# Optimization experiments

Hardware: AMD Instinct MI355X
Metric: run time of the kernel (lower is better)

Reference implementation:

```python
import jax, jax.numpy as jnp
import numpy as np

Q = 12          # hidden_features = number of qubits
L = 3           # spectrum_layer
NBLK = 2        # N sequential circuit blocks
IMG = 32        # image side; input_dim = IMG*IMG = 1024
DIM = 1 << Q

# bit table: BITS[s, j] = bit of wire j (wire 0 = most significant) in basis state s
_s = np.arange(DIM)
_BITS_NP = np.stack([(_s >> (Q - 1 - j)) & 1 for j in range(Q)], axis=1).astype(np.float32)
BITS = jnp.asarray(_BITS_NP)                      # (2^Q, Q)
ZVALS = jnp.asarray(1.0 - 2.0 * _BITS_NP)         # PauliZ eigenvalues per wire

def _cz_ring_sign(r):
    # diagonal of a ring of CZ gates on pairs (j, (j+r) % Q); CZ is diagonal, ring commutes
    m = sum(_BITS_NP[:, j] * _BITS_NP[:, (j + r) % Q] for j in range(Q))
    return jnp.asarray(1.0 - 2.0 * (m % 2)).astype(np.float32)

# StronglyEntanglingLayers default ranges for 2 sub-layers: r = (l % (Q-1)) + 1 -> [1, 2]
CZ_SIGNS = [_cz_ring_sign(1), _cz_ring_sign(2)]

def _rot(phi, theta, omega):
    # PennyLane Rot(phi, theta, omega) = RZ(omega) RY(theta) RZ(phi)
    c = jnp.cos(theta * 0.5).astype(jnp.complex64)
    s = jnp.sin(theta * 0.5).astype(jnp.complex64)
    row0 = jnp.stack([jnp.exp(-0.5j * (phi + omega)) * c, -jnp.exp(0.5j * (phi - omega)) * s])
    row1 = jnp.stack([jnp.exp(0.5j * (omega - phi)) * s, jnp.exp(0.5j * (phi + omega)) * c])
    return jnp.stack([row0, row1])  # (2,2) complex64

def _apply_1q(st, U, wire):
    b = st.shape[0]
    left, right = 1 << wire, 1 << (Q - 1 - wire)
    st = st.reshape(b, left, 2, right)
    st = jnp.einsum('ij,bljr->blir', U, st)
    return st.reshape(b, DIM)

def _circuit(inputs, w):
    # inputs: (b, Q) real angles; w: (L, 2, Q, 3)
    b = inputs.shape[0]
    st = jnp.zeros((b, DIM), jnp.complex64).at[:, 0].set(1.0)
    # RZ(theta) = diag(e^{-i t/2}, e^{+i t/2}) on every wire -> one diagonal phase per sample
    enc = jnp.exp(1j * (inputs @ (BITS - 0.5).T)).astype(jnp.complex64)  # (b, 2^Q)
    for i in range(L):
        st = st * enc
        for l in range(2):
            for wire in range(Q):
                st = _apply_1q(st, _rot(w[i, l, wire, 0], w[i, l, wire, 1], w[i, l, wire, 2]), wire)
            st = st * CZ_SIGNS[l]
    probs = st.real * st.real + st.imag * st.imag
    return probs @ ZVALS  # (b, Q) expval PauliZ per wire

def setup_inputs() -> dict:
    key = jax.random.key(0)
    ks = jax.random.split(key, 6)
    return {
        'x': jax.random.normal(ks[0], (2048, 1, IMG, IMG), jnp.float32),
        'conv_w': jax.random.normal(ks[1], (Q, 1, 3, 3), jnp.float32) * 0.3,
        'conv_b': jax.random.normal(ks[2], (Q,), jnp.float32) * 0.1,
        'weights1': jax.random.normal(ks[3], (NBLK, L, 2, Q, 3), jnp.float32) * 0.4,
        'lin_w': jax.random.normal(ks[4], (IMG * IMG, Q), jnp.float32) * 0.2,
        'lin_b': jax.random.normal(ks[5], (IMG * IMG,), jnp.float32) * 0.05,
    }

def reference(x, conv_w, conv_b, weights1, lin_w, lin_b):
    b = x.shape[0]
    y = jax.lax.conv_general_dilated(
        x, conv_w, window_strides=(2, 2), padding=((1, 1), (1, 1)),
        dimension_numbers=('NCHW', 'OIHW', 'NCHW')) + conv_b[None, :, None, None]
    xr = y.reshape(b, Q, -1).mean(axis=2)  # global average pool per channel -> (b, Q)
    for n in range(NBLK):
        xr = _circuit(xr, weights1[n])
    out = xr @ lin_w.T + lin_b
    return out.reshape(b, 1, IMG, IMG)
```

## Files before the change

kernel.cpp:

```cpp
#include <hip/hip_runtime.h>

typedef float vf2  __attribute__((ext_vector_type(2)));
typedef float v128f __attribute__((ext_vector_type(128)));

__device__ __forceinline__ vf2 cmulv(vf2 a, vf2 b){
  vf2 br; br.x = -b.y; br.y = b.x;
  return a.x*b + a.y*br;
}

#define ROWS 66
#define FENCE() asm volatile("" ::: "memory")

#define ALPHA(d, j) (((d) & 1) \
  ? (W[((((d)>>1)*2+1)*12+(j))*3+0] + W[((((d)>>1)*2+0)*12+(j))*3+2]) \
  : (W[((((d)>>1)*2+0)*12+(j))*3+0] + xr[(j)] + W[(((((d)>>1)-1)*2+1)*12+(j))*3+2]))

#define GATES6(sl, par) do{ \
  _Pragma("unroll") \
  for (int lb = 0; lb < 6; lb++){ \
    const int wire_ = (par) ? (5 - lb) : (11 - lb); \
    const float t_ = scsl[(sl)*12 + wire_].y; \
    _Pragma("unroll") \
    for (int w0 = 0; w0 < 64; w0++){ \
      if (w0 & (1 << lb)) continue; \
      const int w1 = w0 | (1 << lb); \
      const float ax_ = st[2*w0], ay_ = st[2*w0+1]; \
      const float bx_ = st[2*w1], by_ = st[2*w1+1]; \
      st[2*w0]   = __builtin_fmaf(-t_, bx_, ax_); \
      st[2*w0+1] = __builtin_fmaf(-t_, by_, ay_); \
      st[2*w1]   = __builtin_fmaf( t_, ax_, bx_); \
      st[2*w1+1] = __builtin_fmaf( t_, ay_, by_); \
    } \
  } \
}while(0)

#define TRANSPOSE() do{ \
  _Pragma("unroll") \
  for (int w = 0; w < 64; w++){ \
    vf2 t_; t_.x = st[2*w]; t_.y = st[2*w+1]; \
    xbuf[w * ROWS + u] = t_; \
  } \
  FENCE(); \
  _Pragma("unroll") \
  for (int j = 0; j < 32; j++){ \
    float4 f_ = ((const float4*)&xbuf[u * ROWS])[j]; \
    st[4*j] = f_.x; st[4*j+1] = f_.y; st[4*j+2] = f_.z; st[4*j+3] = f_.w; \
  } \
  FENCE(); \
}while(0)

#define DIAG(d, par) do{ \
  vf2 lp_ = ltab[(d)-1][u]; \
  vf2 lpn_ = -lp_; \
  const unsigned m_ = (par) ? ( ((u >> 5) & 1u) | ((u & 1u) << 5) ) \
                            : ( (((u >> 1) & 1u) << 5) | ((u & 1u) << 4) \
                              | (((u >> 5) & 1u) << 1) | ((u >> 4) & 1u) ); \
  _Pragma("unroll") \
  for (int w = 0; w < 64; w++){ \
    vf2 dph_ = tabs[(d)-1][w]; \
    const int sx_ = __popc((unsigned)w & m_) & 1; \
    vf2 a_; a_.x = st[2*w]; a_.y = st[2*w+1]; \
    vf2 t_ = cmulv(a_, dph_); \
    vf2 r_ = cmulv(t_, sx_ ? lpn_ : lp_); \
    st[2*w] = r_.x; st[2*w+1] = r_.y; \
  } \
}while(0)

__global__ __attribute__((amdgpu_flat_work_group_size(64,64)))
__attribute__((amdgpu_waves_per_eu(1)))
void qiddm_wave(const float* __restrict__ gx,
                const float* __restrict__ gcw,
                const float* __restrict__ gcb,
                const float* __restrict__ gw1,
                const float* __restrict__ glw,
                const float* __restrict__ glb,
                float* __restrict__ gout)
{
  __shared__ vf2 xbuf[64 * ROWS];
  __shared__ vf2 tabs[5][64];
  __shared__ vf2 ltab[5][64];
  __shared__ vf2 scsl[72];

  const int u = threadIdx.x;
  const int bid = blockIdx.x;

  float xr[12];

  {
    float* img = (float*)xbuf;
#pragma unroll
    for (int i = 0; i < 4; i++){
      float4 q4 = ((const float4*)gx)[(size_t)bid * 256 + i * 64 + u];
      ((float4*)img)[i * 64 + u] = q4;
    }
    float p[4][9];
#pragma unroll
    for (int i = 0; i < 4; i++){
      int pos = u + 64 * i, oi = pos >> 4, oj = pos & 15;
#pragma unroll
      for (int ki = 0; ki < 3; ki++)
#pragma unroll
        for (int kj = 0; kj < 3; kj++){
          int ri = 2*oi - 1 + ki, cj = 2*oj - 1 + kj;
          p[i][ki*3+kj] = (ri >= 0 && ri < 32 && cj >= 0 && cj < 32) ? img[ri*32+cj] : 0.0f;
        }
    }
#pragma unroll
    for (int q = 0; q < 12; q++){
      float a = 0.0f;
#pragma unroll
      for (int e = 0; e < 9; e++){
        float wv = gcw[q*9+e];
#pragma unroll
        for (int i = 0; i < 4; i++) a += p[i][e] * wv;
      }
#pragma unroll
      for (int off = 32; off; off >>= 1) a += __shfl_xor(a, off);
      xr[q] = gcb[q] + a * (1.0f/256.0f);
    }
  }

#pragma unroll 1
  for (int n = 0; n < 2; n++){
    const float* W = gw1 + n * 216;

    float myc = 1.0f;
#pragma unroll
    for (int rep = 0; rep < 2; rep++){
      int e = u + rep * 64;
      if (e < 72){
        float sv, cv; __sincosf(0.5f * W[e*3+1], &sv, &cv);
        vf2 ct; ct.x = cv; ct.y = __fdividef(sv, cv); scsl[e] = ct;
        if (e >= 12) myc *= cv;
      }
    }
#pragma unroll
    for (int off = 32; off; off >>= 1) myc *= __shfl_xor(myc, off);
    const float C2 = myc * myc;

#pragma unroll
    for (int d = 1; d <= 5; d++){
      const int par = d & 1;
      const int r = par ? 1 : 2;
      {
        float ph = 0.0f;
#pragma unroll
        for (int lb = 0; lb < 6; lb++){
          int wire = par ? (5 - lb) : (11 - lb);
          ph += ALPHA(d, wire) * ((float)((u >> lb) & 1) - 0.5f);
        }
        int idx_r = par ? (u << 6) : u;
        int y = ((idx_r << r) | (idx_r >> (12 - r))) & 0xFFF;
        int s = __popc(idx_r & y) & 1;
        float sv, cv; __sincosf(ph, &sv, &cv);
        vf2 e_; e_.x = cv; e_.y = sv; if (s) e_ = -e_;
        tabs[d-1][u] = e_;
      }
      {
        float ph = 0.0f;
#pragma unroll
        for (int lb = 0; lb < 6; lb++){
          int wire = par ? (11 - lb) : (5 - lb);
          ph += ALPHA(d, wire) * ((float)((u >> lb) & 1) - 0.5f);
        }
        int idx_l = par ? u : (u << 6);
        int y = ((idx_l << r) | (idx_l >> (12 - r))) & 0xFFF;
        int s = __popc(idx_l & y) & 1;
        float sv, cv; __sincosf(ph, &sv, &cv);
        vf2 e_; e_.x = cv; e_.y = sv; if (s) e_ = -e_;
        ltab[d-1][u] = e_;
      }
    }
    FENCE();

    v128f st;
    float fl = 1.0f;
#pragma unroll
    for (int lb = 0; lb < 6; lb++){
      vf2 ct = scsl[11 - lb];
      fl *= ((u >> lb) & 1) ? (ct.x * ct.y) : ct.x;
    }
    float qc[6], qs[6];
#pragma unroll
    for (int rb = 0; rb < 6; rb++){
      vf2 ct = scsl[5 - rb]; qc[rb] = ct.x; qs[rb] = ct.x * ct.y;
    }
#pragma unroll
    for (int w = 0; w < 64; w++){
      float Qw =  ((w & 1)  ? qs[0] : qc[0]);
      Qw      *=  ((w & 2)  ? qs[1] : qc[1]);
      Qw      *=  ((w & 4)  ? qs[2] : qc[2]);
      Qw      *=  ((w & 8)  ? qs[3] : qc[3]);
      Qw      *=  ((w & 16) ? qs[4] : qc[4]);
      Qw      *=  ((w & 32) ? qs[5] : qc[5]);
      st[2*w] = fl * Qw; st[2*w+1] = 0.0f;
    }

#pragma unroll 1
    for (int k = 2; k < 12; k++){
      const int sl  = k >> 1;
      const int par = ((k + 1) >> 1) & 1;
      if (k & 1) TRANSPOSE();
      else       DIAG(sl, par);
      GATES6(sl, par);
    }

    {
      float P = 0.f, mm[6] = {0.f,0.f,0.f,0.f,0.f,0.f};
#pragma unroll
      for (int w = 0; w < 64; w++){
        float re = st[2*w], im = st[2*w+1];
        float pr = re*re + im*im;
        P += pr;
#pragma unroll
        for (int i = 0; i < 6; i++)
          mm[i] += ((w >> (5 - i)) & 1) ? -pr : pr;
      }
#pragma unroll
      for (int q = 0; q < 12; q++){
        float val = (q < 6) ? (((u >> (5 - q)) & 1) ? -P : P)
                            : mm[q - 6];
#pragma unroll
        for (int off = 32; off; off >>= 1) val += __shfl_xor(val, off);
        xr[q] = val * C2;
      }
    }
  }

  {
#pragma unroll
    for (int i = 0; i < 16; i++){
      int o = i * 64 + u;
      const float4* wr = (const float4*)(glw + o * 12);
      float4 w0 = wr[0], w1 = wr[1], w2 = wr[2];
      float a = glb[o];
      a += xr[0]*w0.x + xr[1]*w0.y + xr[2]*w0.z + xr[3]*w0.w;
      a += xr[4]*w1.x + xr[5]*w1.y + xr[6]*w1.z + xr[7]*w1.w;
      a += xr[8]*w2.x + xr[9]*w2.y + xr[10]*w2.z + xr[11]*w2.w;
      gout[(size_t)bid * 1024 + o] = a;
    }
  }
}

extern "C" void kernel_launch(void* const* d_in, const int* in_sizes, int n_in,
                              void* d_out, int out_size, void* d_ws, size_t ws_size,
                              hipStream_t stream)
{
  (void)n_in; (void)d_ws; (void)ws_size; (void)out_size;
  const float* x  = (const float*)d_in[0];
  const float* cw = (const float*)d_in[1];
  const float* cb = (const float*)d_in[2];
  const float* w1 = (const float*)d_in[3];
  const float* lw = (const float*)d_in[4];
  const float* lb = (const float*)d_in[5];
  float* out = (float*)d_out;
  const int nb = in_sizes[0] / 1024;
  hipLaunchKernelGGL(qiddm_wave, dim3(nb), dim3(64), 0, stream,
                     x, cw, cb, w1, lw, lb, out);
}
```

Measured before the change: 182.9 us.

## Process two samples per wave and share the sample-independent first circuit stage

Each 64-lane block now simulates two samples (A and B) with two register-resident state vectors, and the grid is halved. The gate stages before the first input-dependent diagonal are the same for both samples, so they are computed once and the state is copied to the second sample. The LDS transpose is split into two half-size buffers, and the phase tables are extended for the second sample. The intent is to cut redundant work and raise instruction-level parallelism, at the cost of doubled register state and fewer waves per CU.

```diff
diff --git a/kernel.cpp b/kernel.cpp
--- a/kernel.cpp
+++ b/kernel.cpp
@@ -11,11 +11,20 @@
 #define ROWS 66
 #define FENCE() asm volatile("" ::: "memory")
 
-#define ALPHA(d, j) (((d) & 1) \
+#define ALPHA(d, j, XR) (((d) & 1) \
   ? (W[((((d)>>1)*2+1)*12+(j))*3+0] + W[((((d)>>1)*2+0)*12+(j))*3+2]) \
-  : (W[((((d)>>1)*2+0)*12+(j))*3+0] + xr[(j)] + W[(((((d)>>1)-1)*2+1)*12+(j))*3+2]))
-
-#define GATES6(sl, par) do{ \
+  : (W[((((d)>>1)*2+0)*12+(j))*3+0] + XR[(j)] + W[(((((d)>>1)-1)*2+1)*12+(j))*3+2]))
+
+#define BFLY(ST, w0i, w1i, t_) do{ \
+  const float ax_=ST[2*(w0i)], ay_=ST[2*(w0i)+1]; \
+  const float bx_=ST[2*(w1i)], by_=ST[2*(w1i)+1]; \
+  ST[2*(w0i)]   = __builtin_fmaf(-(t_), bx_, ax_); \
+  ST[2*(w0i)+1] = __builtin_fmaf(-(t_), by_, ay_); \
+  ST[2*(w1i)]   = __builtin_fmaf( (t_), ax_, bx_); \
+  ST[2*(w1i)+1] = __builtin_fmaf( (t_), ay_, by_); \
+}while(0)
+
+#define GATES6_1(ST, sl, par) do{ \
   _Pragma("unroll") \
   for (int lb = 0; lb < 6; lb++){ \
     const int wire_ = (par) ? (5 - lb) : (11 - lb); \
@@ -24,45 +33,152 @@
     for (int w0 = 0; w0 < 64; w0++){ \
       if (w0 & (1 << lb)) continue; \
       const int w1 = w0 | (1 << lb); \
-      const float ax_ = st[2*w0], ay_ = st[2*w0+1]; \
-      const float bx_ = st[2*w1], by_ = st[2*w1+1]; \
-      st[2*w0]   = __builtin_fmaf(-t_, bx_, ax_); \
-      st[2*w0+1] = __builtin_fmaf(-t_, by_, ay_); \
-      st[2*w1]   = __builtin_fmaf( t_, ax_, bx_); \
-      st[2*w1+1] = __builtin_fmaf( t_, ay_, by_); \
+      BFLY(ST, w0, w1, t_); \
     } \
   } \
 }while(0)
 
-#define TRANSPOSE() do{ \
+#define GATES6_2(sl, par) do{ \
+  _Pragma("unroll") \
+  for (int lb = 0; lb < 6; lb++){ \
+    const int wire_ = (par) ? (5 - lb) : (11 - lb); \
+    const float t_ = scsl[(sl)*12 + wire_].y; \
+    _Pragma("unroll") \
+    for (int w0 = 0; w0 < 64; w0++){ \
+      if (w0 & (1 << lb)) continue; \
+      const int w1 = w0 | (1 << lb); \
+      BFLY(stA, w0, w1, t_); \
+      BFLY(stB, w0, w1, t_); \
+    } \
+  } \
+}while(0)
+
+#define TRANSPOSE_S(ST, XB) do{ \
+  if (u < 32){ \
+    _Pragma("unroll") \
+    for (int w = 32; w < 64; w++){ vf2 t_; t_.x = ST[2*w]; t_.y = ST[2*w+1]; \
+      XB[(w-32) * ROWS + u] = t_; } \
+  } else { \
+    _Pragma("unroll") \
+    for (int w = 0; w < 32; w++){ vf2 t_; t_.x = ST[2*w]; t_.y = ST[2*w+1]; \
+      XB[w * ROWS + u] = t_; } \
+  } \
+  FENCE(); \
+  if (u < 32){ \
+    _Pragma("unroll") \
+    for (int t = 0; t < 16; t++){ \
+      float4 f_ = ((const float4*)&XB[u * ROWS + 32])[t]; \
+      ST[64+4*t] = f_.x; ST[64+4*t+1] = f_.y; ST[64+4*t+2] = f_.z; ST[64+4*t+3] = f_.w; } \
+  } else { \
+    _Pragma("unroll") \
+    for (int t = 0; t < 16; t++){ \
+      float4 f_ = ((const float4*)&XB[(u-32) * ROWS])[t]; \
+      ST[4*t] = f_.x; ST[4*t+1] = f_.y; ST[4*t+2] = f_.z; ST[4*t+3] = f_.w; } \
+  } \
+  FENCE(); \
+  if (u < 32){ \
+    _Pragma("unroll") \
+    for (int w = 0; w < 32; w++){ vf2 t_; t_.x = ST[2*w]; t_.y = ST[2*w+1]; \
+      XB[w * ROWS + u] = t_; } \
+  } else { \
+    _Pragma("unroll") \
+    for (int w = 32; w < 64; w++){ vf2 t_; t_.x = ST[2*w]; t_.y = ST[2*w+1]; \
+      XB[(w-32) * ROWS + u] = t_; } \
+  } \
+  FENCE(); \
+  if (u < 32){ \
+    _Pragma("unroll") \
+    for (int t = 0; t < 16; t++){ \
+      float4 f_ = ((const float4*)&XB[u * ROWS])[t]; \
+      ST[4*t] = f_.x; ST[4*t+1] = f_.y; ST[4*t+2] = f_.z; ST[4*t+3] = f_.w; } \
+  } else { \
+    _Pragma("unroll") \
+    for (int t = 0; t < 16; t++){ \
+      float4 f_ = ((const float4*)&XB[(u-32) * ROWS + 32])[t]; \
+      ST[64+4*t] = f_.x; ST[64+4*t+1] = f_.y; ST[64+4*t+2] = f_.z; ST[64+4*t+3] = f_.w; } \
+  } \
+  FENCE(); \
+}while(0)
+
+#define TRANSPOSE2() do{ \
+  if (u < 32){ \
+    _Pragma("unroll") \
+    for (int w = 32; w < 64; w++){ vf2 tA_, tB_; \
+      tA_.x = stA[2*w]; tA_.y = stA[2*w+1]; xbA[(w-32) * ROWS + u] = tA_; \
+      tB_.x = stB[2*w]; tB_.y = stB[2*w+1]; xbB[(w-32) * ROWS + u] = tB_; } \
+  } else { \
+    _Pragma("unroll") \
+    for (int w = 0; w < 32; w++){ vf2 tA_, tB_; \
+      tA_.x = stA[2*w]; tA_.y = stA[2*w+1]; xbA[w * ROWS + u] = tA_; \
+      tB_.x = stB[2*w]; tB_.y = stB[2*w+1]; xbB[w * ROWS + u] = tB_; } \
+  } \
+  FENCE(); \
+  if (u < 32){ \
+    _Pragma("unroll") \
+    for (int t = 0; t < 16; t++){ \
+      float4 fA_ = ((const float4*)&xbA[u * ROWS + 32])[t]; \
+      float4 fB_ = ((const float4*)&xbB[u * ROWS + 32])[t]; \
+      stA[64+4*t] = fA_.x; stA[64+4*t+1] = fA_.y; stA[64+4*t+2] = fA_.z; stA[64+4*t+3] = fA_.w; \
+      stB[64+4*t] = fB_.x; stB[64+4*t+1] = fB_.y; stB[64+4*t+2] = fB_.z; stB[64+4*t+3] = fB_.w; } \
+  } else { \
+    _Pragma("unroll") \
+    for (int t = 0; t < 16; t++){ \
+      float4 fA_ = ((const float4*)&xbA[(u-32) * ROWS])[t]; \
+      float4 fB_ = ((const float4*)&xbB[(u-32) * ROWS])[t]; \
+      stA[4*t] = fA_.x; stA[4*t+1] = fA_.y; stA[4*t+2] = fA_.z; stA[4*t+3] = fA_.w; \
+      stB[4*t] = fB_.x; stB[4*t+1] = fB_.y; stB[4*t+2] = fB_.z; stB[4*t+3] = fB_.w; } \
+  } \
+  FENCE(); \
+  if (u < 32){ \
+    _Pragma("unroll") \
+    for (int w = 0; w < 32; w++){ vf2 tA_, tB_; \
+      tA_.x = stA[2*w]; tA_.y = stA[2*w+1]; xbA[w * ROWS + u] = tA_; \
+      tB_.x = stB[2*w]; tB_.y = stB[2*w+1]; xbB[w * ROWS + u] = tB_; } \
+  } else { \
+    _Pragma("unroll") \
+    for (int w = 32; w < 64; w++){ vf2 tA_, tB_; \
+      tA_.x = stA[2*w]; tA_.y = stA[2*w+1]; xbA[(w-32) * ROWS + u] = tA_; \
+      tB_.x = stB[2*w]; tB_.y = stB[2*w+1]; xbB[(w-32) * ROWS + u] = tB_; } \
+  } \
+  FENCE(); \
+  if (u < 32){ \
+    _Pragma("unroll") \
+    for (int t = 0; t < 16; t++){ \
+      float4 fA_ = ((const float4*)&xbA[u * ROWS])[t]; \
+      float4 fB_ = ((const float4*)&xbB[u * ROWS])[t]; \
+      stA[4*t] = fA_.x; stA[4*t+1] = fA_.y; stA[4*t+2] = fA_.z; stA[4*t+3] = fA_.w; \
+      stB[4*t] = fB_.x; stB[4*t+1] = fB_.y; stB[4*t+2] = fB_.z; stB[4*t+3] = fB_.w; } \
+  } else { \
+    _Pragma("unroll") \
+    for (int t = 0; t < 16; t++){ \
+      float4 fA_ = ((const float4*)&xbA[(u-32) * ROWS + 32])[t]; \
+      float4 fB_ = ((const float4*)&xbB[(u-32) * ROWS + 32])[t]; \
+      stA[64+4*t] = fA_.x; stA[64+4*t+1] = fA_.y; stA[64+4*t+2] = fA_.z; stA[64+4*t+3] = fA_.w; \
+      stB[64+4*t] = fB_.x; stB[64+4*t+1] = fB_.y; stB[64+4*t+2] = fB_.z; stB[64+4*t+3] = fB_.w; } \
+  } \
+  FENCE(); \
+}while(0)
+
+#define DIAG2(d) do{ \
+  const int par_ = (d) & 1; \
+  vf2 lpA_ = ((d)==2) ? lA[1] : ((d)==3) ? lA[2] : ((d)==4) ? lA[3] : lA[4]; \
+  vf2 lpB_ = ((d)==2) ? lB[1] : ((d)==3) ? lA[2] : ((d)==4) ? lB[3] : lA[4]; \
+  vf2 lpnA_ = -lpA_, lpnB_ = -lpB_; \
+  const vf2* tA_ = &tabs[(d)-1][0]; \
+  const vf2* tB_ = par_ ? tA_ : &tabsE[((d)>>1)-1][0]; \
+  const unsigned m_ = par_ ? ( ((u >> 5) & 1u) | ((u & 1u) << 5) ) \
+                           : ( (((u >> 1) & 1u) << 5) | ((u & 1u) << 4) \
+                             | (((u >> 5) & 1u) << 1) | ((u >> 4) & 1u) ); \
   _Pragma("unroll") \
   for (int w = 0; w < 64; w++){ \
-    vf2 t_; t_.x = st[2*w]; t_.y = st[2*w+1]; \
-    xbuf[w * ROWS + u] = t_; \
-  } \
-  FENCE(); \
-  _Pragma("unroll") \
-  for (int j = 0; j < 32; j++){ \
-    float4 f_ = ((const float4*)&xbuf[u * ROWS])[j]; \
-    st[4*j] = f_.x; st[4*j+1] = f_.y; st[4*j+2] = f_.z; st[4*j+3] = f_.w; \
-  } \
-  FENCE(); \
-}while(0)
-
-#define DIAG(d, par) do{ \
-  vf2 lp_ = ltab[(d)-1][u]; \
-  vf2 lpn_ = -lp_; \
-  const unsigned m_ = (par) ? ( ((u >> 5) & 1u) | ((u & 1u) << 5) ) \
-                            : ( (((u >> 1) & 1u) << 5) | ((u & 1u) << 4) \
-                              | (((u >> 5) & 1u) << 1) | ((u >> 4) & 1u) ); \
-  _Pragma("unroll") \
-  for (int w = 0; w < 64; w++){ \
-    vf2 dph_ = tabs[(d)-1][w]; \
     const int sx_ = __popc((unsigned)w & m_) & 1; \
-    vf2 a_; a_.x = st[2*w]; a_.y = st[2*w+1]; \
-    vf2 t_ = cmulv(a_, dph_); \
-    vf2 r_ = cmulv(t_, sx_ ? lpn_ : lp_); \
-    st[2*w] = r_.x; st[2*w+1] = r_.y; \
+    vf2 dA_ = tA_[w], dB_ = tB_[w]; \
+    { vf2 a_; a_.x = stA[2*w]; a_.y = stA[2*w+1]; \
+      vf2 t_ = cmulv(a_, dA_); vf2 r_ = cmulv(t_, sx_ ? lpnA_ : lpA_); \
+      stA[2*w] = r_.x; stA[2*w+1] = r_.y; } \
+    { vf2 a_; a_.x = stB[2*w]; a_.y = stB[2*w+1]; \
+      vf2 t_ = cmulv(a_, dB_); vf2 r_ = cmulv(t_, sx_ ? lpnB_ : lpB_); \
+      stB[2*w] = r_.x; stB[2*w+1] = r_.y; } \
   } \
 }while(0)
 
@@ -76,24 +192,30 @@
                 const float* __restrict__ glb,
                 float* __restrict__ gout)
 {
-  __shared__ vf2 xbuf[64 * ROWS];
+  __shared__ vf2 xbA[32 * ROWS];
+  __shared__ vf2 xbB[32 * ROWS];
   __shared__ vf2 tabs[5][64];
-  __shared__ vf2 ltab[5][64];
+  __shared__ vf2 tabsE[2][64];
   __shared__ vf2 scsl[72];
 
   const int u = threadIdx.x;
   const int bid = blockIdx.x;
-
-  float xr[12];
+  const int sid0 = bid * 2, sid1 = bid * 2 + 1;
+
+  float xrA[12], xrB[12];
 
   {
-    float* img = (float*)xbuf;
+    float* imgA = (float*)xbA;
+    float* imgB = (float*)xbB;
 #pragma unroll
     for (int i = 0; i < 4; i++){
-      float4 q4 = ((const float4*)gx)[(size_t)bid * 256 + i * 64 + u];
-      ((float4*)img)[i * 64 + u] = q4;
-    }
-    float p[4][9];
+      float4 qA = ((const float4*)gx)[(size_t)sid0 * 256 + i * 64 + u];
+      float4 qB = ((const float4*)gx)[(size_t)sid1 * 256 + i * 64 + u];
+      ((float4*)imgA)[i * 64 + u] = qA;
+      ((float4*)imgB)[i * 64 + u] = qB;
+    }
+    FENCE();
+    float pA[4][9], pB[4][9];
 #pragma unroll
     for (int i = 0; i < 4; i++){
       int pos = u + 64 * i, oi = pos >> 4, oj = pos & 15;
@@ -102,21 +224,25 @@
 #pragma unroll
         for (int kj = 0; kj < 3; kj++){
           int ri = 2*oi - 1 + ki, cj = 2*oj - 1 + kj;
-          p[i][ki*3+kj] = (ri >= 0 && ri < 32 && cj >= 0 && cj < 32) ? img[ri*32+cj] : 0.0f;
+          const bool ok = (ri >= 0 && ri < 32 && cj >= 0 && cj < 32);
+          const int ix = ri*32+cj;
+          pA[i][ki*3+kj] = ok ? imgA[ix] : 0.0f;
+          pB[i][ki*3+kj] = ok ? imgB[ix] : 0.0f;
         }
     }
 #pragma unroll
     for (int q = 0; q < 12; q++){
-      float a = 0.0f;
+      float aA = 0.0f, aB = 0.0f;
 #pragma unroll
       for (int e = 0; e < 9; e++){
         float wv = gcw[q*9+e];
 #pragma unroll
-        for (int i = 0; i < 4; i++) a += p[i][e] * wv;
-      }
-#pragma unroll
-      for (int off = 32; off; off >>= 1) a += __shfl_xor(a, off);
-      xr[q] = gcb[q] + a * (1.0f/256.0f);
+        for (int i = 0; i < 4; i++){ aA += pA[i][e] * wv; aB += pB[i][e] * wv; }
+      }
+#pragma unroll
+      for (int off = 32; off; off >>= 1){ aA += __shfl_xor(aA, off); aB += __shfl_xor(aB, off); }
+      xrA[q] = gcb[q] + aA * (1.0f/256.0f);
+      xrB[q] = gcb[q] + aB * (1.0f/256.0f);
     }
   }
 
@@ -138,42 +264,59 @@
     for (int off = 32; off; off >>= 1) myc *= __shfl_xor(myc, off);
     const float C2 = myc * myc;
 
+    vf2 lA[5], lB[5];
 #pragma unroll
     for (int d = 1; d <= 5; d++){
       const int par = d & 1;
       const int r = par ? 1 : 2;
       {
-        float ph = 0.0f;
+        float phA = 0.0f, phB = 0.0f;
 #pragma unroll
         for (int lb = 0; lb < 6; lb++){
           int wire = par ? (5 - lb) : (11 - lb);
-          ph += ALPHA(d, wire) * ((float)((u >> lb) & 1) - 0.5f);
+          const float bit = (float)((u >> lb) & 1) - 0.5f;
+          phA += ALPHA(d, wire, xrA) * bit;
+          if (!par) phB += ALPHA(d, wire, xrB) * bit;
         }
         int idx_r = par ? (u << 6) : u;
         int y = ((idx_r << r) | (idx_r >> (12 - r))) & 0xFFF;
         int s = __popc(idx_r & y) & 1;
-        float sv, cv; __sincosf(ph, &sv, &cv);
-        vf2 e_; e_.x = cv; e_.y = sv; if (s) e_ = -e_;
-        tabs[d-1][u] = e_;
+        float sv, cv; __sincosf(phA, &sv, &cv);
+        vf2 eA; eA.x = cv; eA.y = sv; if (s) eA = -eA;
+        tabs[d-1][u] = eA;
+        if (!par){
+          __sincosf(phB, &sv, &cv);
+          vf2 eB; eB.x = cv; eB.y = sv; if (s) eB = -eB;
+          tabsE[(d>>1)-1][u] = eB;
+        }
       }
       {
-        float ph = 0.0f;
+        float phA = 0.0f, phB = 0.0f;
 #pragma unroll
         for (int lb = 0; lb < 6; lb++){
           int wire = par ? (11 - lb) : (5 - lb);
-          ph += ALPHA(d, wire) * ((float)((u >> lb) & 1) - 0.5f);
+          const float bit = (float)((u >> lb) & 1) - 0.5f;
+          phA += ALPHA(d, wire, xrA) * bit;
+          if (!par) phB += ALPHA(d, wire, xrB) * bit;
         }
         int idx_l = par ? u : (u << 6);
         int y = ((idx_l << r) | (idx_l >> (12 - r))) & 0xFFF;
         int s = __popc(idx_l & y) & 1;
-        float sv, cv; __sincosf(ph, &sv, &cv);
-        vf2 e_; e_.x = cv; e_.y = sv; if (s) e_ = -e_;
-        ltab[d-1][u] = e_;
+        float sv, cv; __sincosf(phA, &sv, &cv);
+        vf2 eA; eA.x = cv; eA.y = sv; if (s) eA = -eA;
+        lA[d-1] = eA;
+        if (!par){
+          __sincosf(phB, &sv, &cv);
+          vf2 eB; eB.x = cv; eB.y = sv; if (s) eB = -eB;
+          lB[d-1] = eB;
+        } else {
+          lB[d-1] = eA;
+        }
       }
     }
     FENCE();
 
-    v128f st;
+    v128f stA, stB;
     float fl = 1.0f;
 #pragma unroll
     for (int lb = 0; lb < 6; lb++){
@@ -193,36 +336,60 @@
       Qw      *=  ((w & 8)  ? qs[3] : qc[3]);
       Qw      *=  ((w & 16) ? qs[4] : qc[4]);
       Qw      *=  ((w & 32) ? qs[5] : qc[5]);
-      st[2*w] = fl * Qw; st[2*w+1] = 0.0f;
-    }
+      stA[2*w] = fl * Qw; stA[2*w+1] = 0.0f;
+    }
+
+    {
+      vf2 lp_ = lA[0], lpn_ = -lp_;
+      const unsigned m_ = ((u >> 5) & 1u) | ((u & 1u) << 5);
+#pragma unroll
+      for (int w = 0; w < 64; w++){
+        const int sx_ = __popc((unsigned)w & m_) & 1;
+        vf2 dph_ = tabs[0][w];
+        vf2 a_; a_.x = stA[2*w]; a_.y = stA[2*w+1];
+        vf2 t_ = cmulv(a_, dph_);
+        vf2 r_ = cmulv(t_, sx_ ? lpn_ : lp_);
+        stA[2*w] = r_.x; stA[2*w+1] = r_.y;
+      }
+    }
+    GATES6_1(stA, 1, 1);
+    TRANSPOSE_S(stA, xbA);
+    GATES6_1(stA, 1, 0);
+    stB = stA;
 
 #pragma unroll 1
-    for (int k = 2; k < 12; k++){
+    for (int k = 4; k < 12; k++){
       const int sl  = k >> 1;
       const int par = ((k + 1) >> 1) & 1;
-      if (k & 1) TRANSPOSE();
-      else       DIAG(sl, par);
-      GATES6(sl, par);
+      if (k & 1) TRANSPOSE2();
+      else       DIAG2(sl);
+      GATES6_2(sl, par);
     }
 
     {
-      float P = 0.f, mm[6] = {0.f,0.f,0.f,0.f,0.f,0.f};
+      float PA = 0.f, PB = 0.f;
+      float mmA[6] = {0,0,0,0,0,0}, mmB[6] = {0,0,0,0,0,0};
 #pragma unroll
       for (int w = 0; w < 64; w++){
-        float re = st[2*w], im = st[2*w+1];
-        float pr = re*re + im*im;
-        P += pr;
-#pragma unroll
-        for (int i = 0; i < 6; i++)
-          mm[i] += ((w >> (5 - i)) & 1) ? -pr : pr;
+        float reA = stA[2*w], imA = stA[2*w+1];
+        float reB = stB[2*w], imB = stB[2*w+1];
+        float prA = reA*reA + imA*imA;
+        float prB = reB*reB + imB*imB;
+        PA += prA; PB += prB;
+#pragma unroll
+        for (int i = 0; i < 6; i++){
+          if ((w >> (5 - i)) & 1){ mmA[i] -= prA; mmB[i] -= prB; }
+          else                   { mmA[i] += prA; mmB[i] += prB; }
+        }
       }
 #pragma unroll
       for (int q = 0; q < 12; q++){
-        float val = (q < 6) ? (((u >> (5 - q)) & 1) ? -P : P)
-                            : mm[q - 6];
-#pragma unroll
-        for (int off = 32; off; off >>= 1) val += __shfl_xor(val, off);
-        xr[q] = val * C2;
+        float vA = (q < 6) ? (((u >> (5 - q)) & 1) ? -PA : PA) : mmA[q - 6];
+        float vB = (q < 6) ? (((u >> (5 - q)) & 1) ? -PB : PB) : mmB[q - 6];
+#pragma unroll
+        for (int off = 32; off; off >>= 1){ vA += __shfl_xor(vA, off); vB += __shfl_xor(vB, off); }
+        xrA[q] = vA * C2;
+        xrB[q] = vB * C2;
       }
     }
   }
@@ -233,11 +400,16 @@
       int o = i * 64 + u;
       const float4* wr = (const float4*)(glw + o * 12);
       float4 w0 = wr[0], w1 = wr[1], w2 = wr[2];
-      float a = glb[o];
-      a += xr[0]*w0.x + xr[1]*w0.y + xr[2]*w0.z + xr[3]*w0.w;
-      a += xr[4]*w1.x + xr[5]*w1.y + xr[6]*w1.z + xr[7]*w1.w;
-      a += xr[8]*w2.x + xr[9]*w2.y + xr[10]*w2.z + xr[11]*w2.w;
-      gout[(size_t)bid * 1024 + o] = a;
+      float b = glb[o];
+      float aA = b, aB = b;
+      aA += xrA[0]*w0.x + xrA[1]*w0.y + xrA[2]*w0.z + xrA[3]*w0.w;
+      aA += xrA[4]*w1.x + xrA[5]*w1.y + xrA[6]*w1.z + xrA[7]*w1.w;
+      aA += xrA[8]*w2.x + xrA[9]*w2.y + xrA[10]*w2.z + xrA[11]*w2.w;
+      aB += xrB[0]*w0.x + xrB[1]*w0.y + xrB[2]*w0.z + xrB[3]*w0.w;
+      aB += xrB[4]*w1.x + xrB[5]*w1.y + xrB[6]*w1.z + xrB[7]*w1.w;
+      aB += xrB[8]*w2.x + xrB[9]*w2.y + xrB[10]*w2.z + xrB[11]*w2.w;
+      gout[(size_t)sid0 * 1024 + o] = aA;
+      gout[(size_t)sid1 * 1024 + o] = aB;
     }
   }
 }
@@ -255,6 +427,6 @@
   const float* lb = (const float*)d_in[5];
   float* out = (float*)d_out;
   const int nb = in_sizes[0] / 1024;
-  hipLaunchKernelGGL(qiddm_wave, dim3(nb), dim3(64), 0, stream,
+  hipLaunchKernelGGL(qiddm_wave, dim3(nb / 2), dim3(64), 0, stream,
                      x, cw, cb, w1, lw, lb, out);
 }
```

Measured after the change: 390.8 us. +113.7%, slower.
